# Kernel optimization log

Measured on AMD Instinct MI355X. Metric: run time of the kernel, lower is better.

## Reference

```python
import jax, jax.numpy as jnp
import numpy as np

T, B = 64, 32
LANG_DIM, ENC_H, EMB_D, MEM_H, MEM_L, MEM_IN, NACT = 14, 256, 32, 512, 4, 288, 8


def setup_inputs() -> dict:
    key = jax.random.key(0)
    ks = jax.random.split(key, 32)
    def n(k, shape, scale=0.02):
        return jax.random.normal(k, shape, jnp.float32) * scale
    z = lambda *s: jnp.zeros(s, jnp.float32)
    inp = {}
    inp["img"] = jax.random.normal(ks[0], (T * B, 3, 99, 99), jnp.float32)
    inp["lang"] = jax.random.normal(ks[1], (T, B, LANG_DIM), jnp.float32)
    inp["done"] = (jax.random.uniform(ks[2], (T, B)) < 0.1).astype(jnp.float32)
    inp["action"] = jax.random.randint(ks[3], (T * B,), 0, NACT)
    inp["enc_h0"] = z(B, ENC_H)
    inp["enc_c0"] = z(B, ENC_H)
    inp["mem_h0"] = z(MEM_L, B, MEM_H)
    inp["mem_c0"] = z(MEM_L, B, MEM_H)
    inp["conv1_w"] = n(ks[4], (16, 3, 9, 9)); inp["conv1_b"] = z(16)
    inp["conv2_w"] = n(ks[5], (32, 16, 3, 3)); inp["conv2_b"] = z(32)
    inp["conv3_w"] = n(ks[6], (32, 32, 3, 3)); inp["conv3_b"] = z(32)
    inp["fc_w"] = n(ks[7], (256, 32 * 7 * 7)); inp["fc_b"] = z(256)
    inp["enc_Wih"] = n(ks[8], (4 * ENC_H, LANG_DIM)); inp["enc_Whh"] = n(ks[9], (4 * ENC_H, ENC_H))
    inp["enc_bih"] = z(4 * ENC_H); inp["enc_bhh"] = z(4 * ENC_H)
    inp["emb_w"] = n(ks[10], (EMB_D, ENC_H)); inp["emb_b"] = z(EMB_D)
    inp["mem_Wih0"] = n(ks[11], (4 * MEM_H, MEM_IN))
    inp["mem_WihR"] = n(ks[12], (MEM_L - 1, 4 * MEM_H, MEM_H))
    inp["mem_Whh"] = n(ks[13], (MEM_L, 4 * MEM_H, MEM_H))
    inp["mem_bih"] = z(MEM_L, 4 * MEM_H); inp["mem_bhh"] = z(MEM_L, 4 * MEM_H)
    inp["actor_w"] = n(ks[14], (NACT, MEM_H), 0.01); inp["actor_b"] = z(NACT)
    inp["critic_w"] = n(ks[15], (1, MEM_H), 0.02); inp["critic_b"] = z(1)
    return inp


def _conv(x, w, b, stride):
    y = jax.lax.conv_general_dilated(x, w, (stride, stride), 'VALID',
                                     dimension_numbers=('NCHW', 'OIHW', 'NCHW'))
    return y + b[None, :, None, None]


def _lstm_cell(x, h, c, Wih, Whh, bih, bhh):
    # PyTorch nn.LSTM gate order: i, f, g, o
    gates = x @ Wih.T + bih + h @ Whh.T + bhh
    i, f, g, o = jnp.split(gates, 4, axis=-1)
    c = jax.nn.sigmoid(f) * c + jax.nn.sigmoid(i) * jnp.tanh(g)
    h = jax.nn.sigmoid(o) * jnp.tanh(c)
    return h, c


def reference(img, lang, done, action, enc_h0, enc_c0, mem_h0, mem_c0,
              conv1_w, conv1_b, conv2_w, conv2_b, conv3_w, conv3_b, fc_w, fc_b,
              enc_Wih, enc_Whh, enc_bih, enc_bhh, emb_w, emb_b,
              mem_Wih0, mem_WihR, mem_Whh, mem_bih, mem_bhh,
              actor_w, actor_b, critic_w, critic_b):
    # ---- image encoder ----
    x = jax.nn.relu(_conv(img, conv1_w, conv1_b, 9))   # (TB,16,11,11)
    x = jax.nn.relu(_conv(x, conv2_w, conv2_b, 1))     # (TB,32,9,9)
    x = jax.nn.relu(_conv(x, conv3_w, conv3_b, 1))     # (TB,32,7,7)
    x = x.reshape(x.shape[0], -1)
    img_h = jax.nn.relu(x @ fc_w.T + fc_b)             # (TB,256)

    # ---- language encoder: per-step masked LSTM scan ----
    def enc_step(carry, xs):
        h, c = carry
        xt, dt = xs
        m = (1.0 - dt)[:, None]
        h, c = _lstm_cell(xt, m * h, m * c, enc_Wih, enc_Whh, enc_bih, enc_bhh)
        return (h, c), h
    _, lang_h = jax.lax.scan(enc_step, (enc_h0, enc_c0), (lang, done))  # (T,B,256)
    lang_e = jax.nn.relu(lang_h.reshape(T * B, ENC_H) @ emb_w.T + emb_b)  # (TB,32)

    hidden = jnp.concatenate([img_h, lang_e], axis=1).reshape(T, B, MEM_IN)

    # ---- memory: 4-layer masked LSTM scan ----
    def mem_step(carry, xs):
        h, c = carry  # each (4,B,512)
        xt, dt = xs
        m = (1.0 - dt)[None, :, None]
        h, c = m * h, m * c
        hs, cs, inp = [], [], xt
        for l in range(MEM_L):
            Wih = mem_Wih0 if l == 0 else mem_WihR[l - 1]
            nh, nc = _lstm_cell(inp, h[l], c[l], Wih, mem_Whh[l], mem_bih[l], mem_bhh[l])
            hs.append(nh); cs.append(nc); inp = nh
        return (jnp.stack(hs), jnp.stack(cs)), inp
    _, out = jax.lax.scan(mem_step, (mem_h0, mem_c0), (hidden, done))  # (T,B,512)
    out = out.reshape(T * B, MEM_H)

    # ---- heads ----
    logits = out @ actor_w.T + actor_b                 # (TB,8)
    logp = jax.nn.log_softmax(logits, axis=-1)
    lp_a = jnp.take_along_axis(logp, action[:, None], axis=1)[:, 0]
    ent = -(jnp.exp(logp) * logp).sum(-1)
    value = out @ critic_w.T + critic_b                # (TB,1)
    return jnp.stack([lp_a, ent, value[:, 0]], axis=-1)  # (TB,3)
```

## Files before the change

kernel.cpp:

```cpp
#include <hip/hip_runtime.h>


typedef __bf16 bf16;
typedef __bf16 bf16x8 __attribute__((ext_vector_type(8)));
typedef int v4i __attribute__((ext_vector_type(4)));
typedef float f32x4v __attribute__((ext_vector_type(4)));
typedef float f32x16v __attribute__((ext_vector_type(16)));
typedef unsigned int u32;

#define SCOPE_AGENT __HIP_MEMORY_SCOPE_AGENT
#define HM_ELEMS (65 * 32 * 512)

#define MFMA_AB(acc_, va_, wa_) \
  asm("s_nop 2\n\tv_mfma_f32_32x32x16_bf16 %0, %1, %2, %0" \
      : "+v"(acc_) : "v"(va_), "a"(wa_))
#define ACC_SYNC(acc_) asm volatile("s_nop 7\n\ts_nop 7" : "+v"(acc_))
#define PIN_A(x_) asm volatile("" : "+a"(x_))

__device__ __forceinline__ float sigf_(float x) {
  x = fminf(fmaxf(x, -30.f), 30.f);
  return 1.f / (1.f + __expf(-x));
}
__device__ __forceinline__ float tanhf_(float x) {
  x = fminf(fmaxf(x, -15.f), 15.f);
  float e = __expf(2.f * x);
  return (e - 1.f) / (e + 1.f);
}

__device__ __forceinline__ void async16(const bf16* g, bf16* l) {
  __builtin_amdgcn_global_load_lds(
      (const __attribute__((address_space(1))) u32*)g,
      (__attribute__((address_space(3))) u32*)l, 16, 0, 0);
}

__device__ __forceinline__ void wait_slots(int* f, int n, int tid) {
  if (tid < 64) {
    while (true) {
      int v = (tid < n) ? __hip_atomic_load(f + tid, __ATOMIC_RELAXED, SCOPE_AGENT) : 1;
      if (__all(v != 0)) break;
      __builtin_amdgcn_s_sleep(2);
    }
  }
}
__device__ __forceinline__ void post_slot(int* f) {
  __hip_atomic_store(f, 1, __ATOMIC_RELAXED, SCOPE_AGENT);
}
__device__ __forceinline__ void store_pair_at(bf16* base, size_t elem_idx, float a, float b) {
  unsigned short lo = __builtin_bit_cast(unsigned short, (bf16)a);
  unsigned short hi = __builtin_bit_cast(unsigned short, (bf16)b);
  u32 pk = (u32)lo | ((u32)hi << 16);
  __hip_atomic_store((u32*)base + (elem_idx >> 1), pk, __ATOMIC_RELAXED, SCOPE_AGENT);
}

template<int KREG, int RDIM, bool PRE>
__device__ void scan_body(const bf16* __restrict__ Wrows, const float* __restrict__ biasf,
    const bf16* __restrict__ xbase, const bf16* __restrict__ hbase, bf16* __restrict__ hout,
    const float* __restrict__ cinit, const float* __restrict__ done,
    int* flag_own, int nslot_own, int* flag_x, int nslot_x, int myslot,
    int u0, int tid, char* smem)
{
  constexpr int KW = KREG * RDIM;
  constexpr int NKS = KW / 64;
  constexpr int NI = RDIM / 16;
  bf16* Abuf = (bf16*)smem;
  float* partial = (float*)(smem + KREG * 32 * RDIM * 2);
  float* cl = partial + 4 * 128 * 33;
  const int lane = tid & 63, wv = tid >> 6;
  const int hsel = lane >> 5, ln31 = lane & 31;
  const int ks0 = wv * NKS;

  v4i Wreg[4][NKS];
#pragma unroll
  for (int g = 0; g < 4; ++g) {
    int row = g * RDIM + u0 + ln31;
#pragma unroll
    for (int ks = 0; ks < NKS; ++ks) {
      Wreg[g][ks] = *(const v4i*)(Wrows + (size_t)row * KW + (ks0 + ks) * 16 + hsel * 8);
      PIN_A(Wreg[g][ks]);
    }
  }
  for (int i = tid; i < 1024; i += 256)
    cl[i] = cinit[(i >> 5) * RDIM + u0 + (i & 31)];

  for (int t = 0; t < 64; ++t) {
    if (t > 0) wait_slots(flag_own + (t - 1) * 16, nslot_own, tid);
    if (nslot_x > 0) wait_slots(flag_x + t * 16, nslot_x, tid);
    __syncthreads();
    for (int i = wv; i < KREG * NI; i += 4) {
      int r = i / NI, ii = i - r * NI;
      const bf16* src = (KREG == 2 && r == 0) ? xbase : hbase;
      async16(src + (size_t)t * 32 * RDIM + ii * 512 + lane * 8,
              Abuf + r * 32 * RDIM + ii * 512);
    }
    __syncthreads();

    const bool dmask = done[t * 32 + ln31] != 0.0f;
    f32x16v acc[4] = {};
#pragma unroll
    for (int ks = 0; ks < NKS; ++ks) {
      int kg = (ks0 + ks) * 16 + hsel * 8;
      int r = kg / RDIM, kk = kg - r * RDIM;
      v4i a = *(const v4i*)(Abuf + r * 32 * RDIM + ln31 * RDIM +
                            ((((kk >> 3) ^ (ln31 & 7)) << 3)));
      if (r == KREG - 1 && dmask) a = v4i{0, 0, 0, 0};
#pragma unroll
      for (int g = 0; g < 4; ++g)
        MFMA_AB(acc[g], a, Wreg[g][ks]);
    }
    ACC_SYNC(acc[0]); ACC_SYNC(acc[1]); ACC_SYNC(acc[2]); ACC_SYNC(acc[3]);
#pragma unroll
    for (int g = 0; g < 4; ++g) {
      float* pp = partial + (wv * 128 + g * 32 + ln31) * 33 + 4 * hsel;
#pragma unroll
      for (int q = 0; q < 4; ++q)
#pragma unroll
        for (int s = 0; s < 4; ++s)
          pp[8 * q + s] = acc[g][4 * q + s];
    }
    __syncthreads();
    for (int p = tid; p < 512; p += 256) {
      int m = p >> 4, up = (p & 15) * 2;
      float dn = done[t * 32 + m];
      float hv[2];
#pragma unroll
      for (int j = 0; j < 2; ++j) {
        int u = up + j;
        float gg[4];
#pragma unroll
        for (int g = 0; g < 4; ++g) {
          int col = g * 32 + u;
          float s = partial[col * 33 + m] + partial[(128 + col) * 33 + m]
                  + partial[(256 + col) * 33 + m] + partial[(384 + col) * 33 + m];
          if (PRE) s += biasf[(size_t)(t * 32 + m) * (4 * RDIM) + g * RDIM + u0 + u];
          else     s += biasf[g * RDIM + u0 + u];
          gg[g] = s;
        }
        int ci = m * 32 + u;
        float cold = cl[ci] * (1.0f - dn);
        float cn = sigf_(gg[1]) * cold + sigf_(gg[0]) * tanhf_(gg[2]);
        cl[ci] = cn;
        hv[j] = sigf_(gg[3]) * tanhf_(cn);
      }
      int k = u0 + up;
      int pos = ((((k >> 3) ^ (m & 7)) << 3)) + (k & 7);
      store_pair_at(hout, ((size_t)(t + 1) * 32 + m) * RDIM + pos, hv[0], hv[1]);
    }
    __syncthreads();
    if (tid == 0) post_slot(flag_own + t * 16 + myslot);
  }
}

__device__ void emb_body(const bf16* __restrict__ Wemb, const float* __restrict__ emb_b,
    const bf16* __restrict__ h_enc, bf16* __restrict__ hidden,
    int* fle, int* flb, int t0, int tid, char* smem)
{
  bf16* Abuf = (bf16*)smem;
  float* partial = (float*)(smem + 32 * 256 * 2);
  const int lane = tid & 63, wv = tid >> 6;
  const int hsel = lane >> 5, ln31 = lane & 31;
  const int ks0 = wv * 4;
  bf16x8 Wreg[4];
#pragma unroll
  for (int ks = 0; ks < 4; ++ks)
    Wreg[ks] = *(const bf16x8*)(Wemb + ln31 * 256 + (ks0 + ks) * 16 + hsel * 8);
  for (int t = t0; t < 64; t += 4) {
    wait_slots(fle + t * 16, 8, tid);
    __syncthreads();
    {
      const uint4* s = (const uint4*)(h_enc + (size_t)(t + 1) * 32 * 256);
      for (int i = tid; i < 1024; i += 256) ((uint4*)Abuf)[i] = s[i];
    }
    __syncthreads();
    f32x16v acc = {};
#pragma unroll
    for (int ks = 0; ks < 4; ++ks) {
      int k = (ks0 + ks) * 16 + hsel * 8;
      bf16x8 a = *(const bf16x8*)(Abuf + ln31 * 256 + ((((k >> 3) ^ (ln31 & 7)) << 3)));
      acc = __builtin_amdgcn_mfma_f32_32x32x16_bf16(a, Wreg[ks], acc, 0, 0, 0);
    }
    float* pp = partial + (wv * 32 + ln31) * 33 + 4 * hsel;
#pragma unroll
    for (int q = 0; q < 4; ++q)
#pragma unroll
      for (int s = 0; s < 4; ++s)
        pp[8 * q + s] = acc[4 * q + s];
    __syncthreads();
    for (int p = tid; p < 512; p += 256) {
      int m = p >> 4, np = (p & 15) * 2;
      float v[2];
#pragma unroll
      for (int j = 0; j < 2; ++j) {
        int col = np + j;
        float s = partial[col * 33 + m] + partial[(32 + col) * 33 + m]
                + partial[(64 + col) * 33 + m] + partial[(96 + col) * 33 + m] + emb_b[col];
        v[j] = fmaxf(s, 0.f);
      }
      int k = 256 + np;
      int pos = ((((k >> 3) ^ (m & 7)) << 3)) + (k & 7);
      store_pair_at(hidden, (size_t)(t * 32 + m) * 512 + pos, v[0], v[1]);
    }
    __syncthreads();
    if (tid == 0) post_slot(flb + t * 16);
  }
}

__device__ void heads_body(const bf16* __restrict__ h3, const float* __restrict__ actor_w,
    const float* __restrict__ actor_b, const float* __restrict__ critic_w,
    const float* __restrict__ critic_b, const int* __restrict__ action,
    float* __restrict__ out, int* fl3, int t0, int tid, char* smem)
{
  float* hS = (float*)smem;
  float* lg = hS + 32 * 520;
  float* vp = lg + 256;
  const int b = tid >> 3, c = tid & 7;
  for (int t = t0; t < 64; t += 8) {
    wait_slots(fl3 + t * 16, 16, tid);
    __syncthreads();
    for (int i = tid; i < 2048; i += 256) {
      int m = i >> 6, j = i & 63;
      bf16x8 v = *(const bf16x8*)(h3 + ((size_t)(t + 1) * 32 + m) * 512 +
                                  ((j ^ (m & 7)) << 3));
#pragma unroll
      for (int q = 0; q < 8; ++q) hS[m * 520 + j * 8 + q] = (float)v[q];
    }
    __syncthreads();
    float acc = actor_b[c];
    float va = 0.f;
#pragma unroll 4
    for (int k = 0; k < 512; k += 4) {
      f32x4v hv = *(const f32x4v*)(hS + b * 520 + k);
      f32x4v wv4 = *(const f32x4v*)(actor_w + c * 512 + k);
      acc += hv[0]*wv4[0] + hv[1]*wv4[1] + hv[2]*wv4[2] + hv[3]*wv4[3];
    }
    for (int k = c * 64; k < c * 64 + 64; k += 4) {
      f32x4v hv = *(const f32x4v*)(hS + b * 520 + k);
      f32x4v wv4 = *(const f32x4v*)(critic_w + k);
      va += hv[0]*wv4[0] + hv[1]*wv4[1] + hv[2]*wv4[2] + hv[3]*wv4[3];
    }
    lg[b * 8 + c] = acc;
    vp[b * 8 + c] = va;
    __syncthreads();
    if (tid < 32) {
      const float* L = lg + tid * 8;
      float mx = L[0];
#pragma unroll
      for (int i = 1; i < 8; ++i) mx = fmaxf(mx, L[i]);
      float s = 0.f;
#pragma unroll
      for (int i = 0; i < 8; ++i) s += __expf(L[i] - mx);
      float lse = mx + __logf(s);
      float ent = 0.f;
#pragma unroll
      for (int i = 0; i < 8; ++i) { float lp = L[i] - lse; ent -= __expf(lp) * lp; }
      int a = action[t * 32 + tid];
      a = a < 0 ? 0 : (a > 7 ? 7 : a);
      float val = critic_b[0];
#pragma unroll
      for (int i = 0; i < 8; ++i) val += vp[tid * 8 + i];
      float* o = out + (size_t)(t * 32 + tid) * 3;
      o[0] = L[a] - lse; o[1] = ent; o[2] = val;
    }
    __syncthreads();
  }
}

struct PipeP {
  const bf16 *Wenc, *Wm0, *Wm1, *Wm2, *Wm3, *Wemb;
  const float *pre_enc, *bc, *done, *emb_b, *enc_c0, *mem_c0;
  bf16 *hidden, *h_enc, *h_mem;
  const float *actor_w, *actor_b, *critic_w, *critic_b;
  const int *action;
  float *out;
  int *fl;
};

__global__ __launch_bounds__(256, 1) void pipeline_kernel(PipeP P) {
  extern __shared__ char smem[];
  const int bid = blockIdx.x, tid = threadIdx.x;
  int* fl = P.fl;
  if (bid < 64) {
    int l = bid >> 4, s = bid & 15, u0 = s * 32;
    bf16* hown = P.h_mem + (size_t)l * HM_ELEMS;
    const bf16* W = (l == 0) ? P.Wm0 : (l == 1) ? P.Wm1 : (l == 2) ? P.Wm2 : P.Wm3;
    const bf16* xb = (l == 0) ? P.hidden : P.h_mem + (size_t)(l - 1) * HM_ELEMS + 32 * 512;
    int* fown = fl + l * 1024;
    int* fx = (l == 0) ? fl + 320 * 16 : fl + (l - 1) * 1024;
    int nx = (l == 0) ? 1 : 16;
    scan_body<2, 512, false>(W, P.bc + l * 2048, xb, hown, hown,
        P.mem_c0 + l * 32 * 512, P.done, fown, 16, fx, nx, s, u0, tid, smem);
  } else if (bid < 72) {
    int s = bid - 64, u0 = s * 32;
    scan_body<1, 256, true>(P.Wenc, P.pre_enc, nullptr, P.h_enc, P.h_enc,
        P.enc_c0, P.done, fl + 256 * 16, 8, nullptr, 0, s, u0, tid, smem);
  } else if (bid < 76) {
    emb_body(P.Wemb, P.emb_b, P.h_enc, P.hidden, fl + 256 * 16, fl + 320 * 16,
             bid - 72, tid, smem);
  } else {
    heads_body(P.h_mem + 3ull * HM_ELEMS, P.actor_w, P.actor_b, P.critic_w, P.critic_b,
        P.action, P.out, fl + 3 * 1024, bid - 76, tid, smem);
  }
}

__device__ __forceinline__ void cvt_store8(bf16* dst, const float* src) {
  f32x4v a = *(const f32x4v*)src, b = *(const f32x4v*)(src + 4);
  bf16x8 o;
#pragma unroll
  for (int j = 0; j < 4; ++j) { o[j] = (bf16)a[j]; o[4 + j] = (bf16)b[j]; }
  *(bf16x8*)dst = o;
}

__global__ void prep_kernel(
    const float* __restrict__ enc_Whh, const float* __restrict__ mem_Wih0,
    const float* __restrict__ mem_WihR, const float* __restrict__ mem_Whh,
    const float* __restrict__ emb_w, const float* __restrict__ mem_bih,
    const float* __restrict__ mem_bhh, const float* __restrict__ enc_h0,
    const float* __restrict__ mem_h0, const float* __restrict__ fc_w,
    const float* __restrict__ conv1_w,
    bf16* __restrict__ Wenc, bf16* __restrict__ Wm0, bf16* __restrict__ Wm123,
    bf16* __restrict__ Wemb, float* __restrict__ bc,
    bf16* __restrict__ h_enc, bf16* __restrict__ h_mem, bf16* __restrict__ fcw_bf,
    bf16* __restrict__ w1bf)
{
  int v = blockIdx.x * 256 + threadIdx.x;
  if (v < 32768) { cvt_store8(Wenc + v * 8, enc_Whh + v * 8); return; }
  v -= 32768;
  if (v < 262144) {
    int col = v >> 7, c = v & 127;
    bf16x8 o = {};
    if (c < 36) {
      const float* s = mem_Wih0 + col * 288 + c * 8;
#pragma unroll
      for (int j = 0; j < 8; ++j) o[j] = (bf16)s[j];
    } else if (c >= 64) {
      const float* s = mem_Whh + col * 512 + (c - 64) * 8;
#pragma unroll
      for (int j = 0; j < 8; ++j) o[j] = (bf16)s[j];
    }
    *(bf16x8*)(Wm0 + (size_t)v * 8) = o;
    return;
  }
  v -= 262144;
  if (v < 786432) {
    int l = v >> 18, r = v & 262143, col = r >> 7, c = r & 127;
    const float* s = (c < 64) ? mem_WihR + ((size_t)(l * 2048 + col)) * 512 + c * 8
                              : mem_Whh + ((size_t)((l + 1) * 2048 + col)) * 512 + (c - 64) * 8;
    cvt_store8(Wm123 + (size_t)v * 8, s);
    return;
  }
  v -= 786432;
  if (v < 1024) { cvt_store8(Wemb + v * 8, emb_w + v * 8); return; }
  v -= 1024;
  if (v < 1024) {
#pragma unroll
    for (int j = 0; j < 8; ++j) bc[v * 8 + j] = mem_bih[v * 8 + j] + mem_bhh[v * 8 + j];
    return;
  }
  v -= 1024;
  if (v < 1024) {
    int m = v >> 5, c = v & 31;
    bf16x8 o;
    const float* s = enc_h0 + m * 256 + c * 8;
#pragma unroll
    for (int j = 0; j < 8; ++j) o[j] = (bf16)s[j];
    *(bf16x8*)(h_enc + m * 256 + ((c ^ (m & 7)) << 3)) = o;
    return;
  }
  v -= 1024;
  if (v < 8192) {
    int l = v >> 11, r = v & 2047, m = r >> 6, c = r & 63;
    bf16x8 o;
    const float* s = mem_h0 + ((size_t)(l * 32 + m)) * 512 + c * 8;
#pragma unroll
    for (int j = 0; j < 8; ++j) o[j] = (bf16)s[j];
    *(bf16x8*)(h_mem + (size_t)l * HM_ELEMS + m * 512 + ((c ^ (m & 7)) << 3)) = o;
    return;
  }
  v -= 8192;
  if (v < 50176) { cvt_store8(fcw_bf + (size_t)v * 8, fc_w + (size_t)v * 8); return; }
  v -= 50176;
  if (v < 512) {
    int oc = v >> 5, c = v & 31;
    bf16x8 o = {};
#pragma unroll
    for (int j = 0; j < 8; ++j) {
      int k = c * 8 + j;
      if (k < 243) o[j] = (bf16)conv1_w[oc * 243 + k];
    }
    *(bf16x8*)(w1bf + v * 8) = o;
    return;
  }
}

__global__ void pre_enc_kernel(const float* __restrict__ lang, const float* __restrict__ Wih,
    const float* __restrict__ bih, const float* __restrict__ bhh, float* __restrict__ pre)
{
  int idx = blockIdx.x * 256 + threadIdx.x;
  if (idx >= 64 * 32 * 1024) return;
  int col = idx & 1023, bm = idx >> 10;
  float acc = bih[col] + bhh[col];
  const float* lp = lang + bm * 14;
  const float* wp = Wih + col * 14;
#pragma unroll
  for (int k = 0; k < 14; ++k) acc += lp[k] * wp[k];
  pre[idx] = acc;
}

__global__ __launch_bounds__(256) void conv1_mfma(const float* __restrict__ img,
    const bf16* __restrict__ w1bf, const float* __restrict__ bias, float* __restrict__ out) {
  __shared__ bf16 sP[128 * 256];
  const int n = blockIdx.x, tid = threadIdx.x;
  const int lane = tid & 63, wv = tid >> 6;
  for (int i = tid; i < 4096; i += 256) ((uint4*)sP)[i] = uint4{0u, 0u, 0u, 0u};
  __syncthreads();
  const float* ib = img + (size_t)n * 29403;
  for (int e = tid; e < 29403; e += 256) {
    int c = e / 9801, r = e - c * 9801;
    int h = r / 99, w = r - h * 99;
    int oh = h / 9, kh = h - oh * 9;
    int ow = w / 9, kw = w - ow * 9;
    int p = oh * 11 + ow;
    int k = c * 81 + kh * 9 + kw;
    sP[p * 256 + (k ^ ((p & 15) * 8))] = (bf16)ib[e];
  }
  __syncthreads();
  const int oc = lane & 15, kg = lane >> 4;
  bf16x8 bfr[8];
#pragma unroll
  for (int ks = 0; ks < 8; ++ks)
    bfr[ks] = *(const bf16x8*)(w1bf + oc * 256 + ks * 32 + kg * 8);
  const float bv = bias[oc];
#pragma unroll
  for (int mt2 = 0; mt2 < 2; ++mt2) {
    int mt = wv * 2 + mt2;
    int p = mt * 16 + (lane & 15);
    f32x4v acc = {};
#pragma unroll
    for (int ks = 0; ks < 8; ++ks) {
      int k0 = ks * 32 + kg * 8;
      bf16x8 a = *(const bf16x8*)(sP + p * 256 + (k0 ^ ((p & 15) * 8)));
      acc = __builtin_amdgcn_mfma_f32_16x16x32_bf16(a, bfr[ks], acc, 0, 0, 0);
    }
#pragma unroll
    for (int s = 0; s < 4; ++s) {
      int pm = mt * 16 + (lane >> 4) * 4 + s;
      if (pm < 121)
        out[((size_t)n * 16 + oc) * 121 + pm] = fmaxf(acc[s] + bv, 0.f);
    }
  }
}

__global__ void conv2_kernel(const float* __restrict__ in, const float* __restrict__ w,
                             const float* __restrict__ bias, float* __restrict__ out) {
  int n = blockIdx.x;
  __shared__ float sIn[16 * 121];
  __shared__ float sW[32 * 144];
  int tid = threadIdx.x;
  for (int i = tid; i < 4608; i += 256) sW[i] = w[i];
  for (int i = tid; i < 1936; i += 256) sIn[i] = in[(size_t)n * 1936 + i];
  __syncthreads();
  for (int task = tid; task < 288; task += 256) {
    int oc = task & 31, oh = task >> 5;
    float acc[9];
    float bv = bias[oc];
#pragma unroll
    for (int ow = 0; ow < 9; ++ow) acc[ow] = bv;
    for (int c = 0; c < 16; ++c) {
      const float* wr = sW + oc * 144 + c * 9;
      float wq[9];
#pragma unroll
      for (int q = 0; q < 9; ++q) wq[q] = wr[q];
#pragma unroll
      for (int kh = 0; kh < 3; ++kh) {
        const float* ir = sIn + c * 121 + (oh + kh) * 11;
        float iv[11];
#pragma unroll
        for (int q = 0; q < 11; ++q) iv[q] = ir[q];
#pragma unroll
        for (int ow = 0; ow < 9; ++ow)
          acc[ow] += wq[kh*3]*iv[ow] + wq[kh*3+1]*iv[ow+1] + wq[kh*3+2]*iv[ow+2];
      }
    }
#pragma unroll
    for (int ow = 0; ow < 9; ++ow)
      out[(size_t)n * 2592 + oc * 81 + oh * 9 + ow] = fmaxf(acc[ow], 0.f);
  }
}

__global__ void conv3_kernel(const float* __restrict__ in, const float* __restrict__ w,
                             const float* __restrict__ bias, float* __restrict__ out) {
  int n = blockIdx.x;
  __shared__ float sIn[32 * 81];
  __shared__ float sW[32 * 288];
  int tid = threadIdx.x;
  for (int i = tid; i < 9216; i += 256) sW[i] = w[i];
  for (int i = tid; i < 2592; i += 256) sIn[i] = in[(size_t)n * 2592 + i];
  __syncthreads();
  for (int task = tid; task < 224; task += 256) {
    int oc = task & 31, oh = task >> 5;
    float acc[7];
    float bv = bias[oc];
#pragma unroll
    for (int ow = 0; ow < 7; ++ow) acc[ow] = bv;
    for (int c = 0; c < 32; ++c) {
      const float* wr = sW + oc * 288 + c * 9;
      float wq[9];
#pragma unroll
      for (int q = 0; q < 9; ++q) wq[q] = wr[q];
#pragma unroll
      for (int kh = 0; kh < 3; ++kh) {
        const float* ir = sIn + c * 81 + (oh + kh) * 9;
        float iv[9];
#pragma unroll
        for (int q = 0; q < 9; ++q) iv[q] = ir[q];
#pragma unroll
        for (int ow = 0; ow < 7; ++ow)
          acc[ow] += wq[kh*3]*iv[ow] + wq[kh*3+1]*iv[ow+1] + wq[kh*3+2]*iv[ow+2];
      }
    }
#pragma unroll
    for (int ow = 0; ow < 7; ++ow)
      out[(size_t)n * 1568 + oc * 49 + oh * 7 + ow] = fmaxf(acc[ow], 0.f);
  }
}

__global__ __launch_bounds__(256) void fc_kernel(const float* __restrict__ a3,
    const bf16* __restrict__ wbf, const float* __restrict__ fc_b, bf16* __restrict__ hidden) {
  __shared__ bf16 sA[64 * 72];
  __shared__ bf16 sB[64 * 72];
  int bid = blockIdx.x, tid = threadIdx.x;
  int rg = bid >> 2, cg = bid & 3;
  int r0 = rg * 64, c0 = cg * 64;
  int lane = tid & 63, wv = tid >> 6, hsel = lane >> 5, ln31 = lane & 31;
  int wm = wv >> 1, wn = wv & 1;
  f32x16v acc = {};
  for (int kb = 0; kb < 1568; kb += 64) {
    __syncthreads();
    for (int i = tid; i < 512; i += 256) {
      int r = i >> 3, kk = (i & 7) * 8;
      int k = kb + kk;
      bf16x8 va = {}, vb = {};
      if (k < 1568) {
        const float* p = a3 + (size_t)(r0 + r) * 1568 + k;
#pragma unroll
        for (int j = 0; j < 8; ++j) va[j] = (bf16)p[j];
        vb = *(const bf16x8*)(wbf + (size_t)(c0 + r) * 1568 + k);
      }
      *(bf16x8*)(sA + r * 72 + kk) = va;
      *(bf16x8*)(sB + r * 72 + kk) = vb;
    }
    __syncthreads();
#pragma unroll
    for (int ks = 0; ks < 4; ++ks) {
      int k = ks * 16 + hsel * 8;
      bf16x8 a = *(const bf16x8*)(sA + (wm * 32 + ln31) * 72 + k);
      bf16x8 b = *(const bf16x8*)(sB + (wn * 32 + ln31) * 72 + k);
      acc = __builtin_amdgcn_mfma_f32_32x32x16_bf16(a, b, acc, 0, 0, 0);
    }
  }
  int cc = c0 + wn * 32 + ln31;
  float bv = fc_b[cc];
#pragma unroll
  for (int q = 0; q < 4; ++q)
#pragma unroll
    for (int s = 0; s < 4; ++s) {
      int m = 8 * q + 4 * hsel + s;
      int row = r0 + wm * 32 + m;
      int b = row & 31;
      int pos = ((((cc >> 3) ^ (b & 7)) << 3)) + (cc & 7);
      hidden[(size_t)row * 512 + pos] = (bf16)fmaxf(acc[4 * q + s] + bv, 0.f);
    }
}

extern "C" void kernel_launch(void* const* d_in, const int* in_sizes, int n_in,
                              void* d_out, int out_size, void* d_ws, size_t ws_size,
                              hipStream_t stream)
{
  const float* img      = (const float*)d_in[0];
  const float* lang     = (const float*)d_in[1];
  const float* done     = (const float*)d_in[2];
  const int*   action   = (const int*)d_in[3];
  const float* enc_h0   = (const float*)d_in[4];
  const float* enc_c0   = (const float*)d_in[5];
  const float* mem_h0   = (const float*)d_in[6];
  const float* mem_c0   = (const float*)d_in[7];
  const float* conv1_w  = (const float*)d_in[8];
  const float* conv1_b  = (const float*)d_in[9];
  const float* conv2_w  = (const float*)d_in[10];
  const float* conv2_b  = (const float*)d_in[11];
  const float* conv3_w  = (const float*)d_in[12];
  const float* conv3_b  = (const float*)d_in[13];
  const float* fc_w     = (const float*)d_in[14];
  const float* fc_b     = (const float*)d_in[15];
  const float* enc_Wih  = (const float*)d_in[16];
  const float* enc_Whh  = (const float*)d_in[17];
  const float* enc_bih  = (const float*)d_in[18];
  const float* enc_bhh  = (const float*)d_in[19];
  const float* emb_w    = (const float*)d_in[20];
  const float* emb_b    = (const float*)d_in[21];
  const float* mem_Wih0 = (const float*)d_in[22];
  const float* mem_WihR = (const float*)d_in[23];
  const float* mem_Whh  = (const float*)d_in[24];
  const float* mem_bih  = (const float*)d_in[25];
  const float* mem_bhh  = (const float*)d_in[26];
  const float* actor_w  = (const float*)d_in[27];
  const float* actor_b  = (const float*)d_in[28];
  const float* critic_w = (const float*)d_in[29];
  const float* critic_b = (const float*)d_in[30];
  float* out = (float*)d_out;
  (void)in_sizes; (void)n_in; (void)out_size; (void)ws_size;

  char* wp = (char*)d_ws;
  auto alloc = [&](size_t b) { char* p = wp; wp += (b + 255) & ~(size_t)255; return p; };
  float* A1     = (float*)alloc(2048ull * 16 * 121 * 4);
  float* A2     = (float*)alloc(2048ull * 32 * 81 * 4);
  bf16*  hidden = (bf16*) alloc(2048ull * 512 * 2);
  float* preenc = (float*)alloc(64ull * 32 * 1024 * 4);
  bf16*  Wenc   = (bf16*) alloc(1024ull * 256 * 2);
  bf16*  Wm0    = (bf16*) alloc(2048ull * 1024 * 2);
  bf16*  Wm123  = (bf16*) alloc(3ull * 2048 * 1024 * 2);
  bf16*  Wemb   = (bf16*) alloc(32ull * 256 * 2);
  float* bc     = (float*)alloc(4ull * 2048 * 4);
  bf16*  h_enc  = (bf16*) alloc(65ull * 32 * 256 * 2);
  bf16*  h_mem  = (bf16*) alloc(4ull * HM_ELEMS * 2);
  bf16*  fcwbf  = (bf16*) alloc(256ull * 1568 * 2);
  bf16*  w1bf   = (bf16*) alloc(16ull * 256 * 2);
  int*   fl     = (int*)  alloc(24576);
  float* A3     = A1;

  hipMemsetAsync(fl, 0, 24576, stream);
  hipMemsetAsync(hidden, 0, 2048ull * 512 * 2, stream);
  prep_kernel<<<4466, 256, 0, stream>>>(enc_Whh, mem_Wih0, mem_WihR, mem_Whh, emb_w,
      mem_bih, mem_bhh, enc_h0, mem_h0, fc_w, conv1_w,
      Wenc, Wm0, Wm123, Wemb, bc, h_enc, h_mem, fcwbf, w1bf);
  pre_enc_kernel<<<8192, 256, 0, stream>>>(lang, enc_Wih, enc_bih, enc_bhh, preenc);
  conv1_mfma<<<2048, 256, 0, stream>>>(img, w1bf, conv1_b, A1);
  conv2_kernel<<<2048, 256, 0, stream>>>(A1, conv2_w, conv2_b, A2);
  conv3_kernel<<<2048, 256, 0, stream>>>(A2, conv3_w, conv3_b, A3);
  fc_kernel<<<128, 256, 0, stream>>>(A3, fcwbf, fc_b, hidden);

  PipeP P;
  P.Wenc = Wenc; P.Wm0 = Wm0; P.Wm1 = Wm123;
  P.Wm2 = Wm123 + 2048ull * 1024; P.Wm3 = Wm123 + 2ull * 2048 * 1024;
  P.Wemb = Wemb; P.pre_enc = preenc; P.bc = bc; P.done = done; P.emb_b = emb_b;
  P.enc_c0 = enc_c0; P.mem_c0 = mem_c0; P.hidden = hidden; P.h_enc = h_enc; P.h_mem = h_mem;
  P.actor_w = actor_w; P.actor_b = actor_b; P.critic_w = critic_w; P.critic_b = critic_b;
  P.action = action; P.out = out; P.fl = fl;

  (void)hipFuncSetAttribute((const void*)pipeline_kernel,
      hipFuncAttributeMaxDynamicSharedMemorySize, 137216);
  pipeline_kernel<<<84, 256, 137216, stream>>>(P);
}
```

Measured before the change: 1.300 ms.

## Fuse conv chain and FC into persistent pipeline kernel overlapping with LSTM scan

```diff
diff --git a/kernel.cpp b/kernel.cpp
--- a/kernel.cpp
+++ b/kernel.cpp
@@ -264,6 +264,182 @@
   }
 }
 
+__device__ void fc_slice(int t, const bf16* __restrict__ a3bf,
+    const bf16* __restrict__ wbf, const float* __restrict__ fc_b,
+    bf16* __restrict__ hidden, int* flb, int tid, char* smem)
+{
+  bf16* sA = (bf16*)smem;
+  bf16* sB = sA + 32 * 112;
+  float* hidF = (float*)(smem + 65536);
+  const int lane = tid & 63, wv = tid >> 6, hsel = lane >> 5, ln31 = lane & 31;
+  f32x16v acc0 = {}, acc1 = {};
+  for (int kb = 0; kb < 1568; kb += 112) {
+    __syncthreads();
+    for (int i = tid; i < 448; i += 256) {
+      int r = i / 14, kk = (i % 14) * 8;
+      *(bf16x8*)(sA + r * 112 + kk) =
+          *(const bf16x8*)(a3bf + ((size_t)(t * 32 + r)) * 1568 + kb + kk);
+    }
+    for (int i = tid; i < 3584; i += 256) {
+      int c = i / 14, kk = (i % 14) * 8;
+      *(bf16x8*)(sB + c * 112 + kk) =
+          *(const bf16x8*)(wbf + (size_t)c * 1568 + kb + kk);
+    }
+    __syncthreads();
+#pragma unroll
+    for (int kt = 0; kt < 7; ++kt) {
+      int k = kt * 16 + hsel * 8;
+      bf16x8 a  = *(const bf16x8*)(sA + ln31 * 112 + k);
+      bf16x8 b0 = *(const bf16x8*)(sB + (wv * 64 + ln31) * 112 + k);
+      bf16x8 b1 = *(const bf16x8*)(sB + (wv * 64 + 32 + ln31) * 112 + k);
+      acc0 = __builtin_amdgcn_mfma_f32_32x32x16_bf16(a, b0, acc0, 0, 0, 0);
+      acc1 = __builtin_amdgcn_mfma_f32_32x32x16_bf16(a, b1, acc1, 0, 0, 0);
+    }
+  }
+  float bv0 = fc_b[wv * 64 + ln31];
+  float bv1 = fc_b[wv * 64 + 32 + ln31];
+#pragma unroll
+  for (int q = 0; q < 4; ++q)
+#pragma unroll
+    for (int s = 0; s < 4; ++s) {
+      int m = 8 * q + 4 * hsel + s;
+      hidF[m * 256 + wv * 64 + ln31]      = fmaxf(acc0[4 * q + s] + bv0, 0.f);
+      hidF[m * 256 + wv * 64 + 32 + ln31] = fmaxf(acc1[4 * q + s] + bv1, 0.f);
+    }
+  __syncthreads();
+  for (int i = tid; i < 4096; i += 256) {
+    int m = i >> 7, j = (i & 127) * 2;
+    int pos = (((j >> 3) ^ (m & 7)) << 3) + (j & 7);
+    store_pair_at(hidden, ((size_t)(t * 32 + m)) * 512 + pos,
+                  hidF[m * 256 + j], hidF[m * 256 + j + 1]);
+  }
+  __syncthreads();
+  if (tid == 0) post_slot(flb + t * 16 + 1);
+}
+
+__device__ void chain_body(int n, const float* __restrict__ img,
+    const bf16* __restrict__ w1bf, const float* __restrict__ c1b,
+    const float* __restrict__ c2w, const float* __restrict__ c2b,
+    const float* __restrict__ c3w, const float* __restrict__ c3b,
+    const bf16* __restrict__ fcwbf, const float* __restrict__ fc_b,
+    bf16* __restrict__ a3bf, bf16* __restrict__ hidden,
+    int* cnt, int* flb, int tid, char* smem)
+{
+  const int lane = tid & 63, wv = tid >> 6;
+  bf16* sP = (bf16*)smem;
+  float* A1L = (float*)(smem + 65536);
+  float* A2L = A1L + 16 * 121;
+  float* A3L = A2L + 32 * 81;
+  for (int i = tid; i < 4096; i += 256) ((uint4*)sP)[i] = uint4{0u, 0u, 0u, 0u};
+  __syncthreads();
+  const float* ib = img + (size_t)n * 29403;
+  for (int e = tid; e < 29403; e += 256) {
+    int c = e / 9801, r = e - c * 9801;
+    int h = r / 99, w = r - h * 99;
+    int oh = h / 9, kh = h - oh * 9;
+    int ow = w / 9, kw = w - ow * 9;
+    int p = oh * 11 + ow;
+    int k = c * 81 + kh * 9 + kw;
+    sP[p * 256 + (k ^ ((p & 15) * 8))] = (bf16)ib[e];
+  }
+  __syncthreads();
+  {
+    const int oc = lane & 15, kg = lane >> 4;
+    bf16x8 bfr[8];
+#pragma unroll
+    for (int ks = 0; ks < 8; ++ks)
+      bfr[ks] = *(const bf16x8*)(w1bf + oc * 256 + ks * 32 + kg * 8);
+    const float bv = c1b[oc];
+#pragma unroll
+    for (int mt2 = 0; mt2 < 2; ++mt2) {
+      int mt = wv * 2 + mt2;
+      int p = mt * 16 + (lane & 15);
+      f32x4v acc = {};
+#pragma unroll
+      for (int ks = 0; ks < 8; ++ks) {
+        int k0 = ks * 32 + kg * 8;
+        bf16x8 a = *(const bf16x8*)(sP + p * 256 + (k0 ^ ((p & 15) * 8)));
+        acc = __builtin_amdgcn_mfma_f32_16x16x32_bf16(a, bfr[ks], acc, 0, 0, 0);
+      }
+#pragma unroll
+      for (int s = 0; s < 4; ++s) {
+        int pm = mt * 16 + (lane >> 4) * 4 + s;
+        if (pm < 121) A1L[oc * 121 + pm] = fmaxf(acc[s] + bv, 0.f);
+      }
+    }
+  }
+  __syncthreads();
+  float* sW2 = (float*)smem;
+  for (int i = tid; i < 4608; i += 256) sW2[i] = c2w[i];
+  __syncthreads();
+  for (int task = tid; task < 288; task += 256) {
+    int oc = task & 31, oh = task >> 5;
+    float acc[9];
+    float bv = c2b[oc];
+#pragma unroll
+    for (int ow = 0; ow < 9; ++ow) acc[ow] = bv;
+    for (int c = 0; c < 16; ++c) {
+      const float* wr = sW2 + oc * 144 + c * 9;
+      float wq[9];
+#pragma unroll
+      for (int q = 0; q < 9; ++q) wq[q] = wr[q];
+#pragma unroll
+      for (int kh = 0; kh < 3; ++kh) {
+        const float* ir = A1L + c * 121 + (oh + kh) * 11;
+        float iv[11];
+#pragma unroll
+        for (int q = 0; q < 11; ++q) iv[q] = ir[q];
+#pragma unroll
+        for (int ow = 0; ow < 9; ++ow)
+          acc[ow] += wq[kh*3]*iv[ow] + wq[kh*3+1]*iv[ow+1] + wq[kh*3+2]*iv[ow+2];
+      }
+    }
+#pragma unroll
+    for (int ow = 0; ow < 9; ++ow)
+      A2L[oc * 81 + oh * 9 + ow] = fmaxf(acc[ow], 0.f);
+  }
+  __syncthreads();
+  float* sW3 = (float*)smem + 4608;
+  for (int i = tid; i < 9216; i += 256) sW3[i] = c3w[i];
+  __syncthreads();
+  for (int task = tid; task < 224; task += 256) {
+    int oc = task & 31, oh = task >> 5;
+    float acc[7];
+    float bv = c3b[oc];
+#pragma unroll
+    for (int ow = 0; ow < 7; ++ow) acc[ow] = bv;
+    for (int c = 0; c < 32; ++c) {
+      const float* wr = sW3 + oc * 288 + c * 9;
+      float wq[9];
+#pragma unroll
+      for (int q = 0; q < 9; ++q) wq[q] = wr[q];
+#pragma unroll
+      for (int kh = 0; kh < 3; ++kh) {
+        const float* ir = A2L + c * 81 + (oh + kh) * 9;
+        float iv[9];
+#pragma unroll
+        for (int q = 0; q < 9; ++q) iv[q] = ir[q];
+#pragma unroll
+        for (int ow = 0; ow < 7; ++ow)
+          acc[ow] += wq[kh*3]*iv[ow] + wq[kh*3+1]*iv[ow+1] + wq[kh*3+2]*iv[ow+2];
+      }
+    }
+#pragma unroll
+    for (int ow = 0; ow < 7; ++ow)
+      A3L[oc * 49 + oh * 7 + ow] = fmaxf(acc[ow], 0.f);
+  }
+  __syncthreads();
+  for (int i = tid; i < 784; i += 256)
+    store_pair_at(a3bf, (size_t)n * 1568 + 2 * i, A3L[2 * i], A3L[2 * i + 1]);
+  __syncthreads();
+  int* lastF = (int*)(smem + 135168);
+  if (tid == 0)
+    *lastF = __hip_atomic_fetch_add(cnt + (n >> 5), 1, __ATOMIC_ACQ_REL, SCOPE_AGENT);
+  __syncthreads();
+  if (*lastF != 31) return;
+  fc_slice(n >> 5, a3bf, fcwbf, fc_b, hidden, flb, tid, smem);
+}
+
 struct PipeP {
   const bf16 *Wenc, *Wm0, *Wm1, *Wm2, *Wm3, *Wemb;
   const float *pre_enc, *bc, *done, *emb_b, *enc_c0, *mem_c0;
@@ -272,6 +448,10 @@
   const int *action;
   float *out;
   int *fl;
+  const float *img, *c1b, *c2w, *c2b, *c3w, *c3b, *fc_b;
+  const bf16 *w1bf, *fcwbf;
+  bf16 *a3bf;
+  int *cnt;
 };
 
 __global__ __launch_bounds__(256, 1) void pipeline_kernel(PipeP P) {
@@ -285,7 +465,7 @@
     const bf16* xb = (l == 0) ? P.hidden : P.h_mem + (size_t)(l - 1) * HM_ELEMS + 32 * 512;
     int* fown = fl + l * 1024;
     int* fx = (l == 0) ? fl + 320 * 16 : fl + (l - 1) * 1024;
-    int nx = (l == 0) ? 1 : 16;
+    int nx = (l == 0) ? 2 : 16;
     scan_body<2, 512, false>(W, P.bc + l * 2048, xb, hown, hown,
         P.mem_c0 + l * 32 * 512, P.done, fown, 16, fx, nx, s, u0, tid, smem);
   } else if (bid < 72) {
@@ -295,9 +475,12 @@
   } else if (bid < 76) {
     emb_body(P.Wemb, P.emb_b, P.h_enc, P.hidden, fl + 256 * 16, fl + 320 * 16,
              bid - 72, tid, smem);
-  } else {
+  } else if (bid < 84) {
     heads_body(P.h_mem + 3ull * HM_ELEMS, P.actor_w, P.actor_b, P.critic_w, P.critic_b,
         P.action, P.out, fl + 3 * 1024, bid - 76, tid, smem);
+  } else {
+    chain_body(bid - 84, P.img, P.w1bf, P.c1b, P.c2w, P.c2b, P.c3w, P.c3b,
+               P.fcwbf, P.fc_b, P.a3bf, P.hidden, P.cnt, fl + 320 * 16, tid, smem);
   }
 }
 
@@ -403,172 +586,6 @@
 #pragma unroll
   for (int k = 0; k < 14; ++k) acc += lp[k] * wp[k];
   pre[idx] = acc;
-}
-
-__global__ __launch_bounds__(256) void conv1_mfma(const float* __restrict__ img,
-    const bf16* __restrict__ w1bf, const float* __restrict__ bias, float* __restrict__ out) {
-  __shared__ bf16 sP[128 * 256];
-  const int n = blockIdx.x, tid = threadIdx.x;
-  const int lane = tid & 63, wv = tid >> 6;
-  for (int i = tid; i < 4096; i += 256) ((uint4*)sP)[i] = uint4{0u, 0u, 0u, 0u};
-  __syncthreads();
-  const float* ib = img + (size_t)n * 29403;
-  for (int e = tid; e < 29403; e += 256) {
-    int c = e / 9801, r = e - c * 9801;
-    int h = r / 99, w = r - h * 99;
-    int oh = h / 9, kh = h - oh * 9;
-    int ow = w / 9, kw = w - ow * 9;
-    int p = oh * 11 + ow;
-    int k = c * 81 + kh * 9 + kw;
-    sP[p * 256 + (k ^ ((p & 15) * 8))] = (bf16)ib[e];
-  }
-  __syncthreads();
-  const int oc = lane & 15, kg = lane >> 4;
-  bf16x8 bfr[8];
-#pragma unroll
-  for (int ks = 0; ks < 8; ++ks)
-    bfr[ks] = *(const bf16x8*)(w1bf + oc * 256 + ks * 32 + kg * 8);
-  const float bv = bias[oc];
-#pragma unroll
-  for (int mt2 = 0; mt2 < 2; ++mt2) {
-    int mt = wv * 2 + mt2;
-    int p = mt * 16 + (lane & 15);
-    f32x4v acc = {};
-#pragma unroll
-    for (int ks = 0; ks < 8; ++ks) {
-      int k0 = ks * 32 + kg * 8;
-      bf16x8 a = *(const bf16x8*)(sP + p * 256 + (k0 ^ ((p & 15) * 8)));
-      acc = __builtin_amdgcn_mfma_f32_16x16x32_bf16(a, bfr[ks], acc, 0, 0, 0);
-    }
-#pragma unroll
-    for (int s = 0; s < 4; ++s) {
-      int pm = mt * 16 + (lane >> 4) * 4 + s;
-      if (pm < 121)
-        out[((size_t)n * 16 + oc) * 121 + pm] = fmaxf(acc[s] + bv, 0.f);
-    }
-  }
-}
-
-__global__ void conv2_kernel(const float* __restrict__ in, const float* __restrict__ w,
-                             const float* __restrict__ bias, float* __restrict__ out) {
-  int n = blockIdx.x;
-  __shared__ float sIn[16 * 121];
-  __shared__ float sW[32 * 144];
-  int tid = threadIdx.x;
-  for (int i = tid; i < 4608; i += 256) sW[i] = w[i];
-  for (int i = tid; i < 1936; i += 256) sIn[i] = in[(size_t)n * 1936 + i];
-  __syncthreads();
-  for (int task = tid; task < 288; task += 256) {
-    int oc = task & 31, oh = task >> 5;
-    float acc[9];
-    float bv = bias[oc];
-#pragma unroll
-    for (int ow = 0; ow < 9; ++ow) acc[ow] = bv;
-    for (int c = 0; c < 16; ++c) {
-      const float* wr = sW + oc * 144 + c * 9;
-      float wq[9];
-#pragma unroll
-      for (int q = 0; q < 9; ++q) wq[q] = wr[q];
-#pragma unroll
-      for (int kh = 0; kh < 3; ++kh) {
-        const float* ir = sIn + c * 121 + (oh + kh) * 11;
-        float iv[11];
-#pragma unroll
-        for (int q = 0; q < 11; ++q) iv[q] = ir[q];
-#pragma unroll
-        for (int ow = 0; ow < 9; ++ow)
-          acc[ow] += wq[kh*3]*iv[ow] + wq[kh*3+1]*iv[ow+1] + wq[kh*3+2]*iv[ow+2];
-      }
-    }
-#pragma unroll
-    for (int ow = 0; ow < 9; ++ow)
-      out[(size_t)n * 2592 + oc * 81 + oh * 9 + ow] = fmaxf(acc[ow], 0.f);
-  }
-}
-
-__global__ void conv3_kernel(const float* __restrict__ in, const float* __restrict__ w,
-                             const float* __restrict__ bias, float* __restrict__ out) {
-  int n = blockIdx.x;
-  __shared__ float sIn[32 * 81];
-  __shared__ float sW[32 * 288];
-  int tid = threadIdx.x;
-  for (int i = tid; i < 9216; i += 256) sW[i] = w[i];
-  for (int i = tid; i < 2592; i += 256) sIn[i] = in[(size_t)n * 2592 + i];
-  __syncthreads();
-  for (int task = tid; task < 224; task += 256) {
-    int oc = task & 31, oh = task >> 5;
-    float acc[7];
-    float bv = bias[oc];
-#pragma unroll
-    for (int ow = 0; ow < 7; ++ow) acc[ow] = bv;
-    for (int c = 0; c < 32; ++c) {
-      const float* wr = sW + oc * 288 + c * 9;
-      float wq[9];
-#pragma unroll
-      for (int q = 0; q < 9; ++q) wq[q] = wr[q];
-#pragma unroll
-      for (int kh = 0; kh < 3; ++kh) {
-        const float* ir = sIn + c * 81 + (oh + kh) * 9;
-        float iv[9];
-#pragma unroll
-        for (int q = 0; q < 9; ++q) iv[q] = ir[q];
-#pragma unroll
-        for (int ow = 0; ow < 7; ++ow)
-          acc[ow] += wq[kh*3]*iv[ow] + wq[kh*3+1]*iv[ow+1] + wq[kh*3+2]*iv[ow+2];
-      }
-    }
-#pragma unroll
-    for (int ow = 0; ow < 7; ++ow)
-      out[(size_t)n * 1568 + oc * 49 + oh * 7 + ow] = fmaxf(acc[ow], 0.f);
-  }
-}
-
-__global__ __launch_bounds__(256) void fc_kernel(const float* __restrict__ a3,
-    const bf16* __restrict__ wbf, const float* __restrict__ fc_b, bf16* __restrict__ hidden) {
-  __shared__ bf16 sA[64 * 72];
-  __shared__ bf16 sB[64 * 72];
-  int bid = blockIdx.x, tid = threadIdx.x;
-  int rg = bid >> 2, cg = bid & 3;
-  int r0 = rg * 64, c0 = cg * 64;
-  int lane = tid & 63, wv = tid >> 6, hsel = lane >> 5, ln31 = lane & 31;
-  int wm = wv >> 1, wn = wv & 1;
-  f32x16v acc = {};
-  for (int kb = 0; kb < 1568; kb += 64) {
-    __syncthreads();
-    for (int i = tid; i < 512; i += 256) {
-      int r = i >> 3, kk = (i & 7) * 8;
-      int k = kb + kk;
-      bf16x8 va = {}, vb = {};
-      if (k < 1568) {
-        const float* p = a3 + (size_t)(r0 + r) * 1568 + k;
-#pragma unroll
-        for (int j = 0; j < 8; ++j) va[j] = (bf16)p[j];
-        vb = *(const bf16x8*)(wbf + (size_t)(c0 + r) * 1568 + k);
-      }
-      *(bf16x8*)(sA + r * 72 + kk) = va;
-      *(bf16x8*)(sB + r * 72 + kk) = vb;
-    }
-    __syncthreads();
-#pragma unroll
-    for (int ks = 0; ks < 4; ++ks) {
-      int k = ks * 16 + hsel * 8;
-      bf16x8 a = *(const bf16x8*)(sA + (wm * 32 + ln31) * 72 + k);
-      bf16x8 b = *(const bf16x8*)(sB + (wn * 32 + ln31) * 72 + k);
-      acc = __builtin_amdgcn_mfma_f32_32x32x16_bf16(a, b, acc, 0, 0, 0);
-    }
-  }
-  int cc = c0 + wn * 32 + ln31;
-  float bv = fc_b[cc];
-#pragma unroll
-  for (int q = 0; q < 4; ++q)
-#pragma unroll
-    for (int s = 0; s < 4; ++s) {
-      int m = 8 * q + 4 * hsel + s;
-      int row = r0 + wm * 32 + m;
-      int b = row & 31;
-      int pos = ((((cc >> 3) ^ (b & 7)) << 3)) + (cc & 7);
-      hidden[(size_t)row * 512 + pos] = (bf16)fmaxf(acc[4 * q + s] + bv, 0.f);
-    }
 }
 
 extern "C" void kernel_launch(void* const* d_in, const int* in_sizes, int n_in,
@@ -611,8 +628,6 @@
 
   char* wp = (char*)d_ws;
   auto alloc = [&](size_t b) { char* p = wp; wp += (b + 255) & ~(size_t)255; return p; };
-  float* A1     = (float*)alloc(2048ull * 16 * 121 * 4);
-  float* A2     = (float*)alloc(2048ull * 32 * 81 * 4);
   bf16*  hidden = (bf16*) alloc(2048ull * 512 * 2);
   float* preenc = (float*)alloc(64ull * 32 * 1024 * 4);
   bf16*  Wenc   = (bf16*) alloc(1024ull * 256 * 2);
@@ -624,19 +639,16 @@
   bf16*  h_mem  = (bf16*) alloc(4ull * HM_ELEMS * 2);
   bf16*  fcwbf  = (bf16*) alloc(256ull * 1568 * 2);
   bf16*  w1bf   = (bf16*) alloc(16ull * 256 * 2);
-  int*   fl     = (int*)  alloc(24576);
-  float* A3     = A1;
-
-  hipMemsetAsync(fl, 0, 24576, stream);
+  bf16*  a3bf   = (bf16*) alloc(2048ull * 1568 * 2);
+  int*   fl     = (int*)  alloc(24832);
+  int*   cnt    = fl + 6144;
+
+  hipMemsetAsync(fl, 0, 24832, stream);
   hipMemsetAsync(hidden, 0, 2048ull * 512 * 2, stream);
   prep_kernel<<<4466, 256, 0, stream>>>(enc_Whh, mem_Wih0, mem_WihR, mem_Whh, emb_w,
       mem_bih, mem_bhh, enc_h0, mem_h0, fc_w, conv1_w,
       Wenc, Wm0, Wm123, Wemb, bc, h_enc, h_mem, fcwbf, w1bf);
   pre_enc_kernel<<<8192, 256, 0, stream>>>(lang, enc_Wih, enc_bih, enc_bhh, preenc);
-  conv1_mfma<<<2048, 256, 0, stream>>>(img, w1bf, conv1_b, A1);
-  conv2_kernel<<<2048, 256, 0, stream>>>(A1, conv2_w, conv2_b, A2);
-  conv3_kernel<<<2048, 256, 0, stream>>>(A2, conv3_w, conv3_b, A3);
-  fc_kernel<<<128, 256, 0, stream>>>(A3, fcwbf, fc_b, hidden);
 
   PipeP P;
   P.Wenc = Wenc; P.Wm0 = Wm0; P.Wm1 = Wm123;
@@ -645,8 +657,11 @@
   P.enc_c0 = enc_c0; P.mem_c0 = mem_c0; P.hidden = hidden; P.h_enc = h_enc; P.h_mem = h_mem;
   P.actor_w = actor_w; P.actor_b = actor_b; P.critic_w = critic_w; P.critic_b = critic_b;
   P.action = action; P.out = out; P.fl = fl;
+  P.img = img; P.c1b = conv1_b; P.c2w = conv2_w; P.c2b = conv2_b;
+  P.c3w = conv3_w; P.c3b = conv3_b; P.fc_b = fc_b;
+  P.w1bf = w1bf; P.fcwbf = fcwbf; P.a3bf = a3bf; P.cnt = cnt;
 
   (void)hipFuncSetAttribute((const void*)pipeline_kernel,
       hipFuncAttributeMaxDynamicSharedMemorySize, 137216);
-  pipeline_kernel<<<84, 256, 137216, stream>>>(P);
-}
+  pipeline_kernel<<<84 + 2048, 256, 137216, stream>>>(P);
+}
```

New measurement: 2.013 ms. 54.8% more time.
